# Performance work log

Hardware: AMD Instinct MI355X
Metric: run time of the kernel (lower is better)

## Reference

```python
import jax, jax.numpy as jnp
import numpy as np


def setup_inputs() -> dict:
    key = jax.random.key(0)
    k0, k1, k2, k3, k4 = jax.random.split(key, 5)
    B, H, W, C = 8, 64, 64, 256
    d = C // 8
    scale = 0.02
    return {
        "inputs": jax.random.normal(k0, (B, H, W, C), dtype=jnp.float32),
        "w_q": jax.random.normal(k1, (C, d), dtype=jnp.float32) * scale,
        "w_k": jax.random.normal(k2, (C, d), dtype=jnp.float32) * scale,
        "w_v": jax.random.normal(k3, (C, C), dtype=jnp.float32) * scale,
        "w_out": jax.random.normal(k4, (C, C), dtype=jnp.float32) * scale,
    }


def reference(inputs, w_q, w_k, w_v, w_out):
    B, H, W, C = inputs.shape
    N = H * W
    x = inputs.reshape(B, N, C)  # 1x1 conv == per-pixel channel matmul
    q = jnp.einsum("bnc,cd->bnd", x, w_q)   # [B, N, C//8]
    k = jnp.einsum("bnc,cd->bnd", x, w_k)   # [B, N, C//8]
    v = jnp.einsum("bnc,ce->bne", x, w_v)   # [B, N, C]
    attn = jax.nn.softmax(jnp.einsum("bnd,bmd->bnm", q, k), axis=-1)  # [B, N, N]
    attended = jnp.einsum("bnm,bme->bne", attn, v)  # [B, N, C]
    out = jnp.einsum("bne,ec->bnc", attended, w_out)
    return inputs + out.reshape(B, H, W, C)
```

## Files before the change

### kernel.cpp

```cpp
#include <hip/hip_runtime.h>
#include <hip/hip_bf16.h>
#include <stdint.h>

typedef __attribute__((ext_vector_type(8))) short short8;
typedef __attribute__((ext_vector_type(8))) unsigned short ushort8;
typedef __attribute__((ext_vector_type(4))) unsigned short ushort4v;
typedef __attribute__((ext_vector_type(4))) unsigned u32x4;
typedef __attribute__((ext_vector_type(2))) float f32x2;
typedef __attribute__((ext_vector_type(4))) float f32x4;
typedef __attribute__((ext_vector_type(16))) float f32x16;

#define B_ 8
#define N_ 4096
#define C_ 256
#define D_ 32
#define LOG2E 1.44269504088896f

__device__ inline unsigned short f2bf(float f) {
  union { float f; unsigned u; } v; v.f = f;
  unsigned r = v.u + 0x7fffu + ((v.u >> 16) & 1u);
  return (unsigned short)(r >> 16);
}
__device__ inline float bf2f(unsigned short u) {
  return __uint_as_float(((unsigned)u) << 16);
}
__device__ inline float exp2_fast(float x) {
  float r; asm("v_exp_f32 %0, %1" : "=v"(r) : "v"(x)); return r;
}
__device__ inline unsigned cvt_pk_bf16(float lo, float hi) {
  unsigned r; asm("v_cvt_pk_bf16_f32 %0, %1, %2" : "=v"(r) : "v"(lo), "v"(hi)); return r;
}
__device__ inline void permlane32_swap(unsigned& a, unsigned& b) {
  asm volatile("v_permlane32_swap_b32 %0, %1" : "+v"(a), "+v"(b));
}
__device__ inline void gll16(const unsigned short* src, void* lds) {
  __builtin_amdgcn_global_load_lds((const __attribute__((address_space(1))) void*)src,
                                   (__attribute__((address_space(3))) void*)lds, 16, 0, 0);
}

__device__ inline size_t wf_addr(int C, int kk) {
  int ct = C >> 4, cl = C & 15, s = kk >> 5, gf = (kk >> 3) & 3, j = kk & 7;
  return ((size_t)((ct * 8 + s) * 64 + gf * 16 + cl)) * 8 + j;
}

__global__ __launch_bounds__(256) void prep_kernel(const float* __restrict__ wq,
                                                   const float* __restrict__ wk,
                                                   const float* __restrict__ wo,
                                                   const float* __restrict__ wv,
                                                   unsigned short* __restrict__ wf,
                                                   unsigned short* __restrict__ wv_b,
                                                   unsigned short* __restrict__ woT_b) {
  int i = blockIdx.x * 256 + threadIdx.x;
  if (i < 16384) {
    int C = i >> 8, kk = i & 255;
    float v = (C < 32) ? wq[kk * 32 + C] * LOG2E : wk[kk * 32 + (C - 32)];
    wf[wf_addr(C, kk)] = f2bf(v);
  } else if (i < 81920) {
    int j = i - 16384;
    wv_b[j] = f2bf(wv[j]);
  } else {
    int j = i - 81920;
    int e2 = j >> 8, e = j & 255;
    woT_b[j] = f2bf(wo[e * 256 + e2]);
  }
}

__global__ __launch_bounds__(256) void prep2_kernel(const unsigned short* __restrict__ woT_b,
                                                    const unsigned short* __restrict__ wv_b,
                                                    unsigned short* __restrict__ wf) {
  const int lane = threadIdx.x & 63, w = threadIdx.x >> 6;
  const int g = lane >> 4, li = lane & 15;
  const int m0 = blockIdx.x * 64 + w * 16;
  const unsigned short* arow = woT_b + (size_t)(m0 + li) * 256 + (g << 3);
  const unsigned short* brow = wv_b + (size_t)li * 256 + (g << 3);
  f32x4 acc[16] = {};
  for (int kk = 0; kk < 256; kk += 32) {
    short8 a = *reinterpret_cast<const short8*>(arow + kk);
#pragma unroll
    for (int ct = 0; ct < 16; ++ct) {
      short8 bb = *reinterpret_cast<const short8*>(brow + (size_t)ct * 16 * 256 + kk);
      acc[ct] = __builtin_amdgcn_mfma_f32_16x16x32_bf16(a, bb, acc[ct], 0, 0, 0);
    }
  }
#pragma unroll
  for (int ct = 0; ct < 16; ++ct)
#pragma unroll
    for (int r = 0; r < 4; ++r) {
      const int C = 64 + m0 + (g << 2) + r;
      const int kk = ct * 16 + li;
      wf[wf_addr(C, kk)] = f2bf(acc[ct][r]);
    }
}

__global__ __launch_bounds__(256, 2) void qkv_kernel(const float* __restrict__ x,
                                                     const unsigned short* __restrict__ wf,
                                                     unsigned short* __restrict__ q,
                                                     unsigned short* __restrict__ k,
                                                     unsigned short* __restrict__ vwT) {
  __shared__ __align__(16) unsigned short xs[64 * 256];
  const int tid = threadIdx.x;
  const int l = tid & 63, w = tid >> 6;
  const int bx = blockIdx.x;
  const int g = l >> 4, li = l & 15;
  const int m0 = bx * 64;

  const unsigned short* wfb = wf + (size_t)(w * 5) * 4096;

  short8 BA[5], BB[5];
#pragma unroll
  for (int c = 0; c < 5; ++c)
    BA[c] = *reinterpret_cast<const short8*>(wfb + ((size_t)(c * 8 + 0) * 64 + l) * 8);
#pragma unroll
  for (int c = 0; c < 5; ++c)
    BB[c] = *reinterpret_cast<const short8*>(wfb + ((size_t)(c * 8 + 1) * 64 + l) * 8);

  {
    const int row = tid >> 2, qtr = tid & 3;
    const float* src = x + (size_t)(m0 + row) * 256 + qtr * 64;
    unsigned short* dstrow = xs + row * 256;
#pragma unroll
    for (int jj = 0; jj < 8; ++jj) {
      f32x4 a0 = *reinterpret_cast<const f32x4*>(src + jj * 8);
      f32x4 a1 = *reinterpret_cast<const f32x4*>(src + jj * 8 + 4);
      union { unsigned u[4]; ushort8 v; } P;
      P.u[0] = cvt_pk_bf16(a0[0], a0[1]); P.u[1] = cvt_pk_bf16(a0[2], a0[3]);
      P.u[2] = cvt_pk_bf16(a1[0], a1[1]); P.u[3] = cvt_pk_bf16(a1[2], a1[3]);
      const int blk = (qtr * 8 + jj) ^ (row & 7);
      *reinterpret_cast<ushort8*>(dstrow + blk * 8) = P.v;
    }
  }
  __syncthreads();

  f32x4 acc[4][5] = {};

#define QSTEP(S, BV, WN, PREF)                                                       \
  {                                                                                  \
    asm volatile("s_waitcnt vmcnt(" WN ")" ::: "memory");                            \
    __builtin_amdgcn_sched_barrier(0);                                               \
    short8 a_[4];                                                                    \
    _Pragma("unroll") for (int mt = 0; mt < 4; ++mt) {                               \
      const int row = mt * 16 + li;                                                  \
      a_[mt] = *reinterpret_cast<const short8*>(                                     \
          xs + row * 256 + ((((S) * 4 + g) ^ (row & 7)) << 3));                      \
    }                                                                                \
    _Pragma("unroll") for (int mt = 0; mt < 4; ++mt)                                 \
        _Pragma("unroll") for (int c = 0; c < 5; ++c)                                \
            acc[mt][c] = __builtin_amdgcn_mfma_f32_16x16x32_bf16(a_[mt], BV[c],      \
                                                                 acc[mt][c], 0, 0, 0); \
    if (PREF) {                                                                      \
      _Pragma("unroll") for (int c = 0; c < 5; ++c)                                  \
          BV[c] = *reinterpret_cast<const short8*>(                                  \
              wfb + ((size_t)(c * 8 + (S) + 2) * 64 + l) * 8);                       \
    }                                                                                \
  }

  QSTEP(0, BA, "5", true)
  QSTEP(1, BB, "5", true)
  QSTEP(2, BA, "5", true)
  QSTEP(3, BB, "5", true)
  QSTEP(4, BA, "5", true)
  QSTEP(5, BB, "5", true)
  QSTEP(6, BA, "5", false)
  QSTEP(7, BB, "0", false)
#undef QSTEP

  const int bb_ = bx >> 6;
#pragma unroll
  for (int mt = 0; mt < 4; ++mt) {
    const int nloc = (bx & 63) * 64 + mt * 16 + (g << 2);
#pragma unroll
    for (int c = 0; c < 5; ++c) {
      const int Cg = w * 5 + c;
      if (Cg < 2) {
        const int col = Cg * 16 + li;
#pragma unroll
        for (int r = 0; r < 4; ++r)
          q[((size_t)bb_ * N_ + nloc + r) * D_ + col] = f2bf(acc[mt][c][r]);
      } else if (Cg < 4) {
        const int col = (Cg - 2) * 16 + li;
#pragma unroll
        for (int r = 0; r < 4; ++r)
          k[((size_t)bb_ * N_ + nloc + r) * D_ + col] = f2bf(acc[mt][c][r]);
      } else {
        const int vc = Cg * 16 + li - 64;
        union { unsigned u[2]; ushort4v v; } P;
        P.u[0] = cvt_pk_bf16(acc[mt][c][0], acc[mt][c][1]);
        P.u[1] = cvt_pk_bf16(acc[mt][c][2], acc[mt][c][3]);
        *reinterpret_cast<ushort4v*>(&vwT[((size_t)bb_ * C_ + vc) * N_ + nloc]) = P.v;
      }
    }
  }
}

__global__ __launch_bounds__(512, 2) void flash_kernel(const unsigned short* __restrict__ q,
                                                       const unsigned short* __restrict__ k,
                                                       const unsigned short* __restrict__ vwT,
                                                       const float* __restrict__ x,
                                                       float* __restrict__ out) {
  __shared__ __align__(16) char smem[147456];
  const int tid = threadIdx.x;
  const int l = tid & 63, w_ = tid >> 6;
  const int kvh = w_ >> 2, gw = w_ & 3;
  const int qg = gw >> 1, ch = gw & 1;
  const int blk = blockIdx.x;
  const int b = blk & 7;
  const int qt = blk >> 3;
  const int h = l >> 5, l31 = l & 31;
  const int R = kvh * 65536;

  const unsigned short* kb_ = k + (size_t)b * N_ * D_;
  const unsigned short* vb_ = vwT + (size_t)b * C_ * N_;

  const int qposb = qt * 128 + qg * 64;
  short8 qb[2][2];
#pragma unroll
  for (int qt2 = 0; qt2 < 2; ++qt2) {
    const size_t qoff = ((size_t)b * N_ + qposb + qt2 * 32 + l31) * D_ + h * 8;
    qb[qt2][0] = *reinterpret_cast<const short8*>(q + qoff);
    qb[qt2][1] = *reinterpret_cast<const short8*>(q + qoff + 16);
  }
  asm volatile("s_waitcnt vmcnt(0)" ::: "memory");

  const int vrow = l >> 3;
  const int vsrc = ((l & 7) ^ ((l >> 3) & 7)) << 3;
  const int krow = l >> 2;
  const int ksrc = ((l & 3) ^ ((l >> 3) & 3)) << 3;
  const int kvbase = kvh * 2048;

#define STAGE(BUF, KV0)                                                           \
  {                                                                               \
    char* vd = smem + R + (BUF) * 32768 + gw * 8192;                              \
    _Pragma("unroll") for (int t = 0; t < 8; ++t)                                 \
        gll16(vb_ + (size_t)(gw * 64 + t * 8 + vrow) * N_ + (KV0) + vsrc,         \
              vd + t * 1024);                                                     \
    gll16(kb_ + (size_t)((KV0) + gw * 16 + krow) * D_ + ksrc,                     \
          smem + 131072 + kvh * 8192 + (BUF) * 4096 + gw * 1024);                 \
  }

  f32x16 o[4][2] = {};
  float lsum[2] = {0.f, 0.f};
  const f32x16 z16 = {};
  const int kkey = (l31 >> 1) & 3;

  STAGE(0, kvbase)

  for (int i = 0; i < 32; ++i) {
    const int buf = i & 1;
    asm volatile("s_waitcnt vmcnt(0)" ::: "memory");
    __builtin_amdgcn_sched_barrier(0);
    __builtin_amdgcn_s_barrier();
    if (i < 31) STAGE(buf ^ 1, kvbase + (i + 1) * 64)
    const char* Vb = smem + R + buf * 32768;
    const char* Kb = smem + 131072 + kvh * 8192 + buf * 4096;
#pragma unroll
    for (int kvt = 0; kvt < 2; ++kvt) {
      const int krow32 = (kvt * 32 + l31) * 64;
      short8 ka0 = *reinterpret_cast<const short8*>(Kb + krow32 + (((0 + h) ^ kkey) << 4));
      short8 ka1 = *reinterpret_cast<const short8*>(Kb + krow32 + (((2 + h) ^ kkey) << 4));
      f32x16 s0 = __builtin_amdgcn_mfma_f32_32x32x16_bf16(ka0, qb[0][0], z16, 0, 0, 0);
      s0 = __builtin_amdgcn_mfma_f32_32x32x16_bf16(ka1, qb[0][1], s0, 0, 0, 0);
      f32x16 s1 = __builtin_amdgcn_mfma_f32_32x32x16_bf16(ka0, qb[1][0], z16, 0, 0, 0);
      s1 = __builtin_amdgcn_mfma_f32_32x32x16_bf16(ka1, qb[1][1], s1, 0, 0, 0);
      short8 pf[2][2];
#pragma unroll
      for (int r = 0; r < 16; ++r) s0[r] = exp2_fast(s0[r]);
      if (ch == 0)
        lsum[0] += (((s0[0] + s0[1]) + (s0[2] + s0[3])) + ((s0[4] + s0[5]) + (s0[6] + s0[7]))) +
                   (((s0[8] + s0[9]) + (s0[10] + s0[11])) + ((s0[12] + s0[13]) + (s0[14] + s0[15])));
      {
        unsigned x0 = cvt_pk_bf16(s0[0], s0[1]),   y0 = cvt_pk_bf16(s0[4], s0[5]);
        unsigned x1 = cvt_pk_bf16(s0[2], s0[3]),   y1 = cvt_pk_bf16(s0[6], s0[7]);
        unsigned x2 = cvt_pk_bf16(s0[8], s0[9]),   y2 = cvt_pk_bf16(s0[12], s0[13]);
        unsigned x3 = cvt_pk_bf16(s0[10], s0[11]), y3 = cvt_pk_bf16(s0[14], s0[15]);
        permlane32_swap(x0, y0); permlane32_swap(x1, y1);
        permlane32_swap(x2, y2); permlane32_swap(x3, y3);
        union U { unsigned u[4]; short8 v; };
        U u0; u0.u[0] = x0; u0.u[1] = x1; u0.u[2] = y0; u0.u[3] = y1;
        U u1; u1.u[0] = x2; u1.u[1] = x3; u1.u[2] = y2; u1.u[3] = y3;
        pf[0][0] = u0.v; pf[0][1] = u1.v;
      }
#pragma unroll
      for (int r = 0; r < 16; ++r) s1[r] = exp2_fast(s1[r]);
      if (ch == 0)
        lsum[1] += (((s1[0] + s1[1]) + (s1[2] + s1[3])) + ((s1[4] + s1[5]) + (s1[6] + s1[7]))) +
                   (((s1[8] + s1[9]) + (s1[10] + s1[11])) + ((s1[12] + s1[13]) + (s1[14] + s1[15])));
      {
        unsigned x0 = cvt_pk_bf16(s1[0], s1[1]),   y0 = cvt_pk_bf16(s1[4], s1[5]);
        unsigned x1 = cvt_pk_bf16(s1[2], s1[3]),   y1 = cvt_pk_bf16(s1[6], s1[7]);
        unsigned x2 = cvt_pk_bf16(s1[8], s1[9]),   y2 = cvt_pk_bf16(s1[12], s1[13]);
        unsigned x3 = cvt_pk_bf16(s1[10], s1[11]), y3 = cvt_pk_bf16(s1[14], s1[15]);
        permlane32_swap(x0, y0); permlane32_swap(x1, y1);
        permlane32_swap(x2, y2); permlane32_swap(x3, y3);
        union U { unsigned u[4]; short8 v; };
        U u0; u0.u[0] = x0; u0.u[1] = x1; u0.u[2] = y0; u0.u[3] = y1;
        U u1; u1.u[0] = x2; u1.u[1] = x3; u1.u[2] = y2; u1.u[3] = y3;
        pf[1][0] = u0.v; pf[1][1] = u1.v;
      }
      __builtin_amdgcn_s_setprio(1);
#pragma unroll
      for (int ct = 0; ct < 4; ++ct) {
        const int rl = ch * 128 + ct * 32 + l31;
        const int vkey = rl & 7;
        const int rb = rl * 128;
        short8 va0 = *reinterpret_cast<const short8*>(Vb + rb + (((kvt * 4 + 0 + h) ^ vkey) << 4));
        short8 va1 = *reinterpret_cast<const short8*>(Vb + rb + (((kvt * 4 + 2 + h) ^ vkey) << 4));
        o[ct][0] = __builtin_amdgcn_mfma_f32_32x32x16_bf16(va0, pf[0][0], o[ct][0], 0, 0, 0);
        o[ct][0] = __builtin_amdgcn_mfma_f32_32x32x16_bf16(va1, pf[0][1], o[ct][0], 0, 0, 0);
        o[ct][1] = __builtin_amdgcn_mfma_f32_32x32x16_bf16(va0, pf[1][0], o[ct][1], 0, 0, 0);
        o[ct][1] = __builtin_amdgcn_mfma_f32_32x32x16_bf16(va1, pf[1][1], o[ct][1], 0, 0, 0);
      }
      __builtin_amdgcn_s_setprio(0);
    }
  }

  lsum[0] += __shfl_xor(lsum[0], 32);
  lsum[1] += __shfl_xor(lsum[1], 32);
  __syncthreads();
  float* lb = reinterpret_cast<float*>(smem + 131072);
  if (ch == 0 && h == 0) {
    lb[kvh * 128 + qg * 64 + l31] = lsum[0];
    lb[kvh * 128 + qg * 64 + 32 + l31] = lsum[1];
  }
  if (kvh == 1) {
    char* ob = smem + gw * 16384;
    int pg = 0;
#pragma unroll
    for (int ct = 0; ct < 4; ++ct)
#pragma unroll
      for (int qt2 = 0; qt2 < 2; ++qt2)
#pragma unroll
        for (int jg = 0; jg < 2; ++jg) {
          u32x4 t;
#pragma unroll
          for (int e = 0; e < 4; ++e) {
            const int j = jg * 4 + e;
            t[e] = cvt_pk_bf16(o[ct][qt2][2 * j], o[ct][qt2][2 * j + 1]);
          }
          *reinterpret_cast<u32x4*>(ob + pg * 1024 + l * 16) = t;
          ++pg;
        }
  }
  __syncthreads();
  if (kvh == 0) {
    float inv[2];
#pragma unroll
    for (int qt2 = 0; qt2 < 2; ++qt2)
      inv[qt2] = 1.0f / (lb[qg * 64 + qt2 * 32 + l31] + lb[128 + qg * 64 + qt2 * 32 + l31]);
    const char* ob = smem + gw * 16384;
    int pg = 0;
#pragma unroll
    for (int ct = 0; ct < 4; ++ct)
#pragma unroll
      for (int qt2 = 0; qt2 < 2; ++qt2)
#pragma unroll
        for (int jg = 0; jg < 2; ++jg) {
          u32x4 t = *reinterpret_cast<const u32x4*>(ob + pg * 1024 + l * 16);
          ++pg;
#pragma unroll
          for (int e = 0; e < 4; ++e) {
            const int j = jg * 4 + e;
            o[ct][qt2][2 * j]     += bf2f((unsigned short)(t[e] & 0xffffu));
            o[ct][qt2][2 * j + 1] += bf2f((unsigned short)(t[e] >> 16));
          }
        }
#pragma unroll
    for (int qt2 = 0; qt2 < 2; ++qt2) {
      const size_t rowbase = ((size_t)b * N_ + qposb + qt2 * 32 + l31) * C_ + ch * 128;
#pragma unroll
      for (int ct = 0; ct < 4; ++ct)
#pragma unroll
        for (int j = 0; j < 8; ++j) {
          const int c = ct * 32 + 2 * (j & 1) + 8 * (j >> 1) + 4 * h;
          f32x2 xr = *reinterpret_cast<const f32x2*>(x + rowbase + c);
          f32x2 t;
          t[0] = o[ct][qt2][2 * j] * inv[qt2] + xr[0];
          t[1] = o[ct][qt2][2 * j + 1] * inv[qt2] + xr[1];
          *reinterpret_cast<f32x2*>(out + rowbase + c) = t;
        }
    }
  }
#undef STAGE
}

extern "C" void kernel_launch(void* const* d_in, const int* in_sizes, int n_in,
                              void* d_out, int out_size, void* d_ws, size_t ws_size,
                              hipStream_t stream) {
  const float* x  = (const float*)d_in[0];
  const float* wq = (const float*)d_in[1];
  const float* wk = (const float*)d_in[2];
  const float* wv = (const float*)d_in[3];
  const float* wo = (const float*)d_in[4];
  float* out = (float*)d_out;
  char* ws = (char*)d_ws;
  unsigned short* wf    = (unsigned short*)(ws + 0);
  unsigned short* wv_b  = (unsigned short*)(ws + 163840);
  unsigned short* woT_b = (unsigned short*)(ws + 294912);
  unsigned short* q     = (unsigned short*)(ws + 425984);
  unsigned short* k     = (unsigned short*)(ws + 2523136);
  unsigned short* vwT   = (unsigned short*)(ws + 4620288);

  prep_kernel<<<576, 256, 0, stream>>>(wq, wk, wo, wv, wf, wv_b, woT_b);
  prep2_kernel<<<4, 256, 0, stream>>>(woT_b, wv_b, wf);
  qkv_kernel<<<512, 256, 0, stream>>>(x, wf, q, k, vwT);
  flash_kernel<<<256, 512, 0, stream>>>(q, k, vwT, x, out);
}
```

Before: 135.7 us.

## Repartition flash warps: each wave owns 32 queries across all channels

Changes the per-wave work split in the flash attention kernel. Before, each wave handled 64 queries times half of the output channels, so QK^T scores and the exp2 were computed twice, once per channel half. Now each of the four waves per KV half owns 32 queries and all 256 output channels. This removes the duplicated score MFMAs and exponentials, but each wave now reads the full V tile from LDS for its 32 queries, so V reads per unit of PV work roughly double. The output accumulator size per wave stays the same.

```diff
diff --git a/kernel.cpp b/kernel.cpp
--- a/kernel.cpp
+++ b/kernel.cpp
@@ -200,8 +200,7 @@
   __shared__ __align__(16) char smem[147456];
   const int tid = threadIdx.x;
   const int l = tid & 63, w_ = tid >> 6;
-  const int kvh = w_ >> 2, gw = w_ & 3;
-  const int qg = gw >> 1, ch = gw & 1;
+  const int kvh = w_ >> 2, qg = w_ & 3;
   const int blk = blockIdx.x;
   const int b = blk & 7;
   const int qt = blk >> 3;
@@ -211,14 +210,10 @@
   const unsigned short* kb_ = k + (size_t)b * N_ * D_;
   const unsigned short* vb_ = vwT + (size_t)b * C_ * N_;
 
-  const int qposb = qt * 128 + qg * 64;
-  short8 qb[2][2];
-#pragma unroll
-  for (int qt2 = 0; qt2 < 2; ++qt2) {
-    const size_t qoff = ((size_t)b * N_ + qposb + qt2 * 32 + l31) * D_ + h * 8;
-    qb[qt2][0] = *reinterpret_cast<const short8*>(q + qoff);
-    qb[qt2][1] = *reinterpret_cast<const short8*>(q + qoff + 16);
-  }
+  const int qposb = qt * 128 + qg * 32;
+  const size_t qoff = ((size_t)b * N_ + qposb + l31) * D_ + h * 8;
+  const short8 qb0 = *reinterpret_cast<const short8*>(q + qoff);
+  const short8 qb1 = *reinterpret_cast<const short8*>(q + qoff + 16);
   asm volatile("s_waitcnt vmcnt(0)" ::: "memory");
 
   const int vrow = l >> 3;
@@ -229,16 +224,16 @@
 
 #define STAGE(BUF, KV0)                                                           \
   {                                                                               \
-    char* vd = smem + R + (BUF) * 32768 + gw * 8192;                              \
+    char* vd = smem + R + (BUF) * 32768 + qg * 8192;                              \
     _Pragma("unroll") for (int t = 0; t < 8; ++t)                                 \
-        gll16(vb_ + (size_t)(gw * 64 + t * 8 + vrow) * N_ + (KV0) + vsrc,         \
+        gll16(vb_ + (size_t)(qg * 64 + t * 8 + vrow) * N_ + (KV0) + vsrc,         \
               vd + t * 1024);                                                     \
-    gll16(kb_ + (size_t)((KV0) + gw * 16 + krow) * D_ + ksrc,                     \
-          smem + 131072 + kvh * 8192 + (BUF) * 4096 + gw * 1024);                 \
-  }
-
-  f32x16 o[4][2] = {};
-  float lsum[2] = {0.f, 0.f};
+    gll16(kb_ + (size_t)((KV0) + qg * 16 + krow) * D_ + ksrc,                     \
+          smem + 131072 + kvh * 8192 + (BUF) * 4096 + qg * 1024);                 \
+  }
+
+  f32x16 o[8] = {};
+  float lsum = 0.f;
   const f32x16 z16 = {};
   const int kkey = (l31 >> 1) & 3;
 
@@ -257,127 +252,91 @@
       const int krow32 = (kvt * 32 + l31) * 64;
       short8 ka0 = *reinterpret_cast<const short8*>(Kb + krow32 + (((0 + h) ^ kkey) << 4));
       short8 ka1 = *reinterpret_cast<const short8*>(Kb + krow32 + (((2 + h) ^ kkey) << 4));
-      f32x16 s0 = __builtin_amdgcn_mfma_f32_32x32x16_bf16(ka0, qb[0][0], z16, 0, 0, 0);
-      s0 = __builtin_amdgcn_mfma_f32_32x32x16_bf16(ka1, qb[0][1], s0, 0, 0, 0);
-      f32x16 s1 = __builtin_amdgcn_mfma_f32_32x32x16_bf16(ka0, qb[1][0], z16, 0, 0, 0);
-      s1 = __builtin_amdgcn_mfma_f32_32x32x16_bf16(ka1, qb[1][1], s1, 0, 0, 0);
-      short8 pf[2][2];
-#pragma unroll
-      for (int r = 0; r < 16; ++r) s0[r] = exp2_fast(s0[r]);
-      if (ch == 0)
-        lsum[0] += (((s0[0] + s0[1]) + (s0[2] + s0[3])) + ((s0[4] + s0[5]) + (s0[6] + s0[7]))) +
-                   (((s0[8] + s0[9]) + (s0[10] + s0[11])) + ((s0[12] + s0[13]) + (s0[14] + s0[15])));
+      f32x16 s = __builtin_amdgcn_mfma_f32_32x32x16_bf16(ka0, qb0, z16, 0, 0, 0);
+      s = __builtin_amdgcn_mfma_f32_32x32x16_bf16(ka1, qb1, s, 0, 0, 0);
+#pragma unroll
+      for (int r = 0; r < 16; ++r) s[r] = exp2_fast(s[r]);
+      lsum += (((s[0] + s[1]) + (s[2] + s[3])) + ((s[4] + s[5]) + (s[6] + s[7]))) +
+              (((s[8] + s[9]) + (s[10] + s[11])) + ((s[12] + s[13]) + (s[14] + s[15])));
+      short8 pf0, pf1;
       {
-        unsigned x0 = cvt_pk_bf16(s0[0], s0[1]),   y0 = cvt_pk_bf16(s0[4], s0[5]);
-        unsigned x1 = cvt_pk_bf16(s0[2], s0[3]),   y1 = cvt_pk_bf16(s0[6], s0[7]);
-        unsigned x2 = cvt_pk_bf16(s0[8], s0[9]),   y2 = cvt_pk_bf16(s0[12], s0[13]);
-        unsigned x3 = cvt_pk_bf16(s0[10], s0[11]), y3 = cvt_pk_bf16(s0[14], s0[15]);
+        unsigned x0 = cvt_pk_bf16(s[0], s[1]),   y0 = cvt_pk_bf16(s[4], s[5]);
+        unsigned x1 = cvt_pk_bf16(s[2], s[3]),   y1 = cvt_pk_bf16(s[6], s[7]);
+        unsigned x2 = cvt_pk_bf16(s[8], s[9]),   y2 = cvt_pk_bf16(s[12], s[13]);
+        unsigned x3 = cvt_pk_bf16(s[10], s[11]), y3 = cvt_pk_bf16(s[14], s[15]);
         permlane32_swap(x0, y0); permlane32_swap(x1, y1);
         permlane32_swap(x2, y2); permlane32_swap(x3, y3);
         union U { unsigned u[4]; short8 v; };
         U u0; u0.u[0] = x0; u0.u[1] = x1; u0.u[2] = y0; u0.u[3] = y1;
         U u1; u1.u[0] = x2; u1.u[1] = x3; u1.u[2] = y2; u1.u[3] = y3;
-        pf[0][0] = u0.v; pf[0][1] = u1.v;
-      }
-#pragma unroll
-      for (int r = 0; r < 16; ++r) s1[r] = exp2_fast(s1[r]);
-      if (ch == 0)
-        lsum[1] += (((s1[0] + s1[1]) + (s1[2] + s1[3])) + ((s1[4] + s1[5]) + (s1[6] + s1[7]))) +
-                   (((s1[8] + s1[9]) + (s1[10] + s1[11])) + ((s1[12] + s1[13]) + (s1[14] + s1[15])));
-      {
-        unsigned x0 = cvt_pk_bf16(s1[0], s1[1]),   y0 = cvt_pk_bf16(s1[4], s1[5]);
-        unsigned x1 = cvt_pk_bf16(s1[2], s1[3]),   y1 = cvt_pk_bf16(s1[6], s1[7]);
-        unsigned x2 = cvt_pk_bf16(s1[8], s1[9]),   y2 = cvt_pk_bf16(s1[12], s1[13]);
-        unsigned x3 = cvt_pk_bf16(s1[10], s1[11]), y3 = cvt_pk_bf16(s1[14], s1[15]);
-        permlane32_swap(x0, y0); permlane32_swap(x1, y1);
-        permlane32_swap(x2, y2); permlane32_swap(x3, y3);
-        union U { unsigned u[4]; short8 v; };
-        U u0; u0.u[0] = x0; u0.u[1] = x1; u0.u[2] = y0; u0.u[3] = y1;
-        U u1; u1.u[0] = x2; u1.u[1] = x3; u1.u[2] = y2; u1.u[3] = y3;
-        pf[1][0] = u0.v; pf[1][1] = u1.v;
+        pf0 = u0.v; pf1 = u1.v;
       }
       __builtin_amdgcn_s_setprio(1);
 #pragma unroll
-      for (int ct = 0; ct < 4; ++ct) {
-        const int rl = ch * 128 + ct * 32 + l31;
+      for (int ct = 0; ct < 8; ++ct) {
+        const int rl = ct * 32 + l31;
         const int vkey = rl & 7;
         const int rb = rl * 128;
         short8 va0 = *reinterpret_cast<const short8*>(Vb + rb + (((kvt * 4 + 0 + h) ^ vkey) << 4));
         short8 va1 = *reinterpret_cast<const short8*>(Vb + rb + (((kvt * 4 + 2 + h) ^ vkey) << 4));
-        o[ct][0] = __builtin_amdgcn_mfma_f32_32x32x16_bf16(va0, pf[0][0], o[ct][0], 0, 0, 0);
-        o[ct][0] = __builtin_amdgcn_mfma_f32_32x32x16_bf16(va1, pf[0][1], o[ct][0], 0, 0, 0);
-        o[ct][1] = __builtin_amdgcn_mfma_f32_32x32x16_bf16(va0, pf[1][0], o[ct][1], 0, 0, 0);
-        o[ct][1] = __builtin_amdgcn_mfma_f32_32x32x16_bf16(va1, pf[1][1], o[ct][1], 0, 0, 0);
+        o[ct] = __builtin_amdgcn_mfma_f32_32x32x16_bf16(va0, pf0, o[ct], 0, 0, 0);
+        o[ct] = __builtin_amdgcn_mfma_f32_32x32x16_bf16(va1, pf1, o[ct], 0, 0, 0);
       }
       __builtin_amdgcn_s_setprio(0);
     }
   }
 
-  lsum[0] += __shfl_xor(lsum[0], 32);
-  lsum[1] += __shfl_xor(lsum[1], 32);
+  lsum += __shfl_xor(lsum, 32);
   __syncthreads();
   float* lb = reinterpret_cast<float*>(smem + 131072);
-  if (ch == 0 && h == 0) {
-    lb[kvh * 128 + qg * 64 + l31] = lsum[0];
-    lb[kvh * 128 + qg * 64 + 32 + l31] = lsum[1];
-  }
+  if (h == 0) lb[kvh * 128 + qg * 32 + l31] = lsum;
   if (kvh == 1) {
-    char* ob = smem + gw * 16384;
+    char* ob = smem + qg * 16384;
     int pg = 0;
 #pragma unroll
-    for (int ct = 0; ct < 4; ++ct)
-#pragma unroll
-      for (int qt2 = 0; qt2 < 2; ++qt2)
-#pragma unroll
-        for (int jg = 0; jg < 2; ++jg) {
-          u32x4 t;
-#pragma unroll
-          for (int e = 0; e < 4; ++e) {
-            const int j = jg * 4 + e;
-            t[e] = cvt_pk_bf16(o[ct][qt2][2 * j], o[ct][qt2][2 * j + 1]);
-          }
-          *reinterpret_cast<u32x4*>(ob + pg * 1024 + l * 16) = t;
-          ++pg;
+    for (int ct = 0; ct < 8; ++ct)
+#pragma unroll
+      for (int jg = 0; jg < 2; ++jg) {
+        u32x4 t;
+#pragma unroll
+        for (int e = 0; e < 4; ++e) {
+          const int j = jg * 4 + e;
+          t[e] = cvt_pk_bf16(o[ct][2 * j], o[ct][2 * j + 1]);
         }
+        *reinterpret_cast<u32x4*>(ob + pg * 1024 + l * 16) = t;
+        ++pg;
+      }
   }
   __syncthreads();
   if (kvh == 0) {
-    float inv[2];
-#pragma unroll
-    for (int qt2 = 0; qt2 < 2; ++qt2)
-      inv[qt2] = 1.0f / (lb[qg * 64 + qt2 * 32 + l31] + lb[128 + qg * 64 + qt2 * 32 + l31]);
-    const char* ob = smem + gw * 16384;
+    const float inv = 1.0f / (lb[qg * 32 + l31] + lb[128 + qg * 32 + l31]);
+    const char* ob = smem + qg * 16384;
     int pg = 0;
 #pragma unroll
-    for (int ct = 0; ct < 4; ++ct)
-#pragma unroll
-      for (int qt2 = 0; qt2 < 2; ++qt2)
-#pragma unroll
-        for (int jg = 0; jg < 2; ++jg) {
-          u32x4 t = *reinterpret_cast<const u32x4*>(ob + pg * 1024 + l * 16);
-          ++pg;
-#pragma unroll
-          for (int e = 0; e < 4; ++e) {
-            const int j = jg * 4 + e;
-            o[ct][qt2][2 * j]     += bf2f((unsigned short)(t[e] & 0xffffu));
-            o[ct][qt2][2 * j + 1] += bf2f((unsigned short)(t[e] >> 16));
-          }
+    for (int ct = 0; ct < 8; ++ct)
+#pragma unroll
+      for (int jg = 0; jg < 2; ++jg) {
+        u32x4 t = *reinterpret_cast<const u32x4*>(ob + pg * 1024 + l * 16);
+        ++pg;
+#pragma unroll
+        for (int e = 0; e < 4; ++e) {
+          const int j = jg * 4 + e;
+          o[ct][2 * j]     += bf2f((unsigned short)(t[e] & 0xffffu));
+          o[ct][2 * j + 1] += bf2f((unsigned short)(t[e] >> 16));
         }
-#pragma unroll
-    for (int qt2 = 0; qt2 < 2; ++qt2) {
-      const size_t rowbase = ((size_t)b * N_ + qposb + qt2 * 32 + l31) * C_ + ch * 128;
-#pragma unroll
-      for (int ct = 0; ct < 4; ++ct)
-#pragma unroll
-        for (int j = 0; j < 8; ++j) {
-          const int c = ct * 32 + 2 * (j & 1) + 8 * (j >> 1) + 4 * h;
-          f32x2 xr = *reinterpret_cast<const f32x2*>(x + rowbase + c);
-          f32x2 t;
-          t[0] = o[ct][qt2][2 * j] * inv[qt2] + xr[0];
-          t[1] = o[ct][qt2][2 * j + 1] * inv[qt2] + xr[1];
-          *reinterpret_cast<f32x2*>(out + rowbase + c) = t;
-        }
-    }
+      }
+    const size_t rowbase = ((size_t)b * N_ + qposb + l31) * C_;
+#pragma unroll
+    for (int ct = 0; ct < 8; ++ct)
+#pragma unroll
+      for (int j = 0; j < 8; ++j) {
+        const int c = ct * 32 + 2 * (j & 1) + 8 * (j >> 1) + 4 * h;
+        f32x2 xr = *reinterpret_cast<const f32x2*>(x + rowbase + c);
+        f32x2 t;
+        t[0] = o[ct][2 * j] * inv + xr[0];
+        t[1] = o[ct][2 * j + 1] * inv + xr[1];
+        *reinterpret_cast<f32x2*>(out + rowbase + c) = t;
+      }
   }
 #undef STAGE
 }
```

Result: faster. 125.4 us (median of 2 runs) (-7.6%).
